# Performance work log

Hardware: AMD Instinct MI355X
Metric: run time of the kernel (lower is better)

The kernel has to match this reference:

```python
import jax, jax.numpy as jnp
import numpy as np

B, N, M = 4, 4096, 4096
EPS = 1e-8
LOG_2PI = float(np.log(2.0 * 3.14159))  # module uses 3.14159, not math.pi


def setup_inputs() -> dict:
    key = jax.random.key(0)
    k1, k2, k3 = jax.random.split(key, 3)
    return {
        "pred_xyz": jax.random.normal(k1, (B, N, 3), dtype=jnp.float32),
        "pred_sigma": jax.random.uniform(k2, (B, N, 2), dtype=jnp.float32),
        "target": jax.random.normal(k3, (B, M, 3), dtype=jnp.float32),
    }


def reference(pred_xyz, pred_sigma, target):
    target_xyz = target[:, :, :3]
    # pairwise squared distances: [B, N, M]
    dist_xy = jnp.sum((pred_xyz[:, :, None, :2] - target_xyz[:, None, :, :2]) ** 2, axis=-1)
    dist_z = (pred_xyz[:, :, None, 2] - target_xyz[:, None, :, 2]) ** 2
    sigma_xy = pred_sigma[:, :, 0:1]  # [B, N, 1]
    sigma_z = pred_sigma[:, :, 1:2]   # [B, N, 1]
    log_coef = -jnp.log(sigma_xy + EPS) - 0.5 * jnp.log(sigma_z + EPS)  # [B, N, 1]
    log_probs = (log_coef - 1.5 * LOG_2PI
                 - 0.5 * dist_xy / (sigma_xy + EPS)
                 - 0.5 * dist_z / (sigma_z + EPS))  # [B, N, M]
    nll = -jax.nn.logsumexp(log_probs, axis=1)  # mixture over N predictions -> [B, M]
    return nll.mean()
```

## Files before the change

### kernel.cpp

```cpp
#include <hip/hip_runtime.h>


constexpr int Bc = 4, Nc = 4096, Mc = 4096;
constexpr int NC = 64;
constexpr int TM = 8;
constexpr int THREADS = 256;
constexpr int MTILE = THREADS * TM;

#define EPS 1e-8f
constexpr float LOG2E   = 1.4426950408889634f;
constexpr float LN2     = 0.6931471805599453f;
constexpr float LOG_2PI = 1.8378762043478343f;
constexpr float K_CONST = -1.5f * LOG_2PI * LOG2E;

__global__ __launch_bounds__(THREADS) void gmm_partial(
    const float* __restrict__ pred_xyz,
    const float* __restrict__ pred_sigma,
    const float* __restrict__ target,
    float* __restrict__ sums)
{
    __shared__ float4 lds[NC * 2];

    const int nck = blockIdx.x;
    const int mt  = blockIdx.y;
    const int b   = blockIdx.z;
    const int tid = threadIdx.x;
    const int n0  = nck * NC;

    if (tid < NC) {
        const int n = n0 + tid;
        const float* pp = pred_xyz + ((size_t)b * Nc + n) * 3;
        const float px = pp[0], py = pp[1], pz = pp[2];
        const float* ps = pred_sigma + ((size_t)b * Nc + n) * 2;
        const float sxy = ps[0] + EPS;
        const float sz  = ps[1] + EPS;
        const float A  = -0.5f * LOG2E * __builtin_amdgcn_rcpf(sxy);
        const float C  = -0.5f * LOG2E * __builtin_amdgcn_rcpf(sz);
        const float k2 = -__builtin_amdgcn_logf(sxy)
                         - 0.5f * __builtin_amdgcn_logf(sz)
                         + K_CONST;
        const float K2 = k2 + A * (px * px + py * py) + C * (pz * pz);
        const float Bx = -2.f * A * px;
        const float By = -2.f * A * py;
        const float Cz = -2.f * C * pz;
        lds[2 * tid]     = make_float4(K2, A, C, Bx);
        lds[2 * tid + 1] = make_float4(By, Cz, 0.f, 0.f);
    }
    __syncthreads();

    float tx[TM], ty[TM], tz[TM], txy2[TM], tz2[TM], acc[TM];
    const int m0 = mt * MTILE;
#pragma unroll
    for (int j = 0; j < TM; ++j) {
        const int m = m0 + j * THREADS + tid;
        const float* tp = target + ((size_t)b * Mc + m) * 3;
        tx[j] = tp[0]; ty[j] = tp[1]; tz[j] = tp[2];
        txy2[j] = tx[j] * tx[j] + ty[j] * ty[j];
        tz2[j]  = tz[j] * tz[j];
        acc[j] = 0.f;
    }

#pragma unroll 4
    for (int i = 0; i < NC; ++i) {
        const float4 r0 = lds[2 * i];
        const float4 r1 = lds[2 * i + 1];
#pragma unroll
        for (int j = 0; j < TM; ++j) {
            float lp = fmaf(r0.y, txy2[j], r0.x);
            lp = fmaf(r0.z, tz2[j], lp);
            lp = fmaf(r0.w, tx[j], lp);
            lp = fmaf(r1.x, ty[j], lp);
            lp = fmaf(r1.y, tz[j], lp);
            acc[j] += __builtin_amdgcn_exp2f(lp);
        }
    }

#pragma unroll
    for (int j = 0; j < TM; ++j) {
        const int m = m0 + j * THREADS + tid;
        atomicAdd(&sums[(size_t)b * Mc + m], acc[j]);
    }
}

__global__ __launch_bounds__(256) void gmm_finalize(
    const float* __restrict__ sums, float* __restrict__ out)
{
    const int i = blockIdx.x * 256 + threadIdx.x;
    float local = __builtin_amdgcn_logf(sums[i]);
#pragma unroll
    for (int off = 32; off > 0; off >>= 1) {
        local += __shfl_down(local, off, 64);
    }
    __shared__ float w[4];
    const int wave = threadIdx.x >> 6;
    if ((threadIdx.x & 63) == 0) w[wave] = local;
    __syncthreads();
    if (threadIdx.x == 0) {
        const float t = w[0] + w[1] + w[2] + w[3];
        atomicAdd(out, -LN2 / (float)(Bc * Mc) * t);
    }
}

extern "C" void kernel_launch(void* const* d_in, const int* in_sizes, int n_in,
                              void* d_out, int out_size, void* d_ws, size_t ws_size,
                              hipStream_t stream) {
    const float* pred_xyz   = (const float*)d_in[0];
    const float* pred_sigma = (const float*)d_in[1];
    const float* target     = (const float*)d_in[2];
    float* out  = (float*)d_out;
    float* sums = (float*)d_ws;

    hipMemsetAsync(sums, 0, (size_t)Bc * Mc * sizeof(float), stream);
    hipMemsetAsync(out, 0, sizeof(float), stream);

    dim3 grid(Nc / NC, Mc / MTILE, Bc);
    gmm_partial<<<grid, THREADS, 0, stream>>>(pred_xyz, pred_sigma, target, sums);
    gmm_finalize<<<Bc * Mc / 256, 256, 0, stream>>>(sums, out);
}
```

Before: 76.74 us.

## Replace atomic accumulation with per-chunk partial buffers and drop memsets

Halves the N chunk size and has each block write its per-target exp-sums to a dedicated partials buffer instead of doing atomicAdd into a shared sums array. The finalize kernel now reduces over all chunks per target before the log. The two memset launches go away, and the output is zeroed inside the first kernel. It also packs the LDS parameters into float4 plus float2 and adds a min-blocks launch bound. The cost is a larger partials workspace (128 chunks x 16K floats) and a heavier finalize pass.

```diff
diff --git a/kernel.cpp b/kernel.cpp
--- a/kernel.cpp
+++ b/kernel.cpp
@@ -2,7 +2,8 @@
 
 
 constexpr int Bc = 4, Nc = 4096, Mc = 4096;
-constexpr int NC = 64;
+constexpr int NC = 32;
+constexpr int NCHUNK = Nc / NC;
 constexpr int TM = 8;
 constexpr int THREADS = 256;
 constexpr int MTILE = THREADS * TM;
@@ -13,19 +14,23 @@
 constexpr float LOG_2PI = 1.8378762043478343f;
 constexpr float K_CONST = -1.5f * LOG_2PI * LOG2E;
 
-__global__ __launch_bounds__(THREADS) void gmm_partial(
+__global__ __launch_bounds__(THREADS, 4) void gmm_partial(
     const float* __restrict__ pred_xyz,
     const float* __restrict__ pred_sigma,
     const float* __restrict__ target,
-    float* __restrict__ sums)
+    float* __restrict__ partials,
+    float* __restrict__ out)
 {
-    __shared__ float4 lds[NC * 2];
+    __shared__ float4 lds4[NC];
+    __shared__ float2 lds2[NC];
 
     const int nck = blockIdx.x;
     const int mt  = blockIdx.y;
     const int b   = blockIdx.z;
     const int tid = threadIdx.x;
     const int n0  = nck * NC;
+
+    if (nck == 0 && mt == 0 && b == 0 && tid == 0) out[0] = 0.f;
 
     if (tid < NC) {
         const int n = n0 + tid;
@@ -43,8 +48,8 @@
         const float Bx = -2.f * A * px;
         const float By = -2.f * A * py;
         const float Cz = -2.f * C * pz;
-        lds[2 * tid]     = make_float4(K2, A, C, Bx);
-        lds[2 * tid + 1] = make_float4(By, Cz, 0.f, 0.f);
+        lds4[tid] = make_float4(K2, A, C, Bx);
+        lds2[tid] = make_float2(By, Cz);
     }
     __syncthreads();
 
@@ -62,8 +67,8 @@
 
 #pragma unroll 4
     for (int i = 0; i < NC; ++i) {
-        const float4 r0 = lds[2 * i];
-        const float4 r1 = lds[2 * i + 1];
+        const float4 r0 = lds4[i];
+        const float2 r1 = lds2[i];
 #pragma unroll
         for (int j = 0; j < TM; ++j) {
             float lp = fmaf(r0.y, txy2[j], r0.x);
@@ -75,29 +80,37 @@
         }
     }
 
+    float* dst = partials + ((size_t)b * NCHUNK + nck) * Mc + m0;
 #pragma unroll
-    for (int j = 0; j < TM; ++j) {
-        const int m = m0 + j * THREADS + tid;
-        atomicAdd(&sums[(size_t)b * Mc + m], acc[j]);
-    }
+    for (int j = 0; j < TM; ++j)
+        dst[j * THREADS + tid] = acc[j];
 }
 
 __global__ __launch_bounds__(256) void gmm_finalize(
-    const float* __restrict__ sums, float* __restrict__ out)
+    const float* __restrict__ partials, float* __restrict__ out)
 {
-    const int i = blockIdx.x * 256 + threadIdx.x;
-    float local = __builtin_amdgcn_logf(sums[i]);
+    const int t = blockIdx.x * 256 + threadIdx.x;
+    const int b = t >> 12;
+    const int m = t & (Mc - 1);
+    const float* src = partials + (size_t)b * NCHUNK * Mc + m;
+
+    float s = 0.f;
+#pragma unroll 8
+    for (int c = 0; c < NCHUNK; ++c)
+        s += src[(size_t)c * Mc];
+
+    float local = __builtin_amdgcn_logf(s);
 #pragma unroll
-    for (int off = 32; off > 0; off >>= 1) {
+    for (int off = 32; off > 0; off >>= 1)
         local += __shfl_down(local, off, 64);
-    }
+
     __shared__ float w[4];
     const int wave = threadIdx.x >> 6;
     if ((threadIdx.x & 63) == 0) w[wave] = local;
     __syncthreads();
     if (threadIdx.x == 0) {
-        const float t = w[0] + w[1] + w[2] + w[3];
-        atomicAdd(out, -LN2 / (float)(Bc * Mc) * t);
+        const float tot = w[0] + w[1] + w[2] + w[3];
+        atomicAdd(out, -LN2 / (float)(Bc * Mc) * tot);
     }
 }
 
@@ -107,13 +120,11 @@
     const float* pred_xyz   = (const float*)d_in[0];
     const float* pred_sigma = (const float*)d_in[1];
     const float* target     = (const float*)d_in[2];
-    float* out  = (float*)d_out;
-    float* sums = (float*)d_ws;
+    float* out      = (float*)d_out;
+    float* partials = (float*)d_ws;
 
-    hipMemsetAsync(sums, 0, (size_t)Bc * Mc * sizeof(float), stream);
-    hipMemsetAsync(out, 0, sizeof(float), stream);
-
-    dim3 grid(Nc / NC, Mc / MTILE, Bc);
-    gmm_partial<<<grid, THREADS, 0, stream>>>(pred_xyz, pred_sigma, target, sums);
-    gmm_finalize<<<Bc * Mc / 256, 256, 0, stream>>>(sums, out);
+    dim3 grid(NCHUNK, Mc / MTILE, Bc);
+    gmm_partial<<<grid, THREADS, 0, stream>>>(pred_xyz, pred_sigma, target,
+                                              partials, out);
+    gmm_finalize<<<Bc * Mc / 256, 256, 0, stream>>>(partials, out);
 }
```

New measurement: 80.80 us. 5.3% more time.
